# Kernel tuning notes

Hardware: AMD Instinct MI355X
Metric: run time of the kernel (lower is better)

The kernel has to match this reference:

```python
import jax, jax.numpy as jnp
import numpy as np

D = 768
H = 8
HD = D // H  # 96
DFF = 2048
EPS = 1e-5


def layernorm(x, g, b):
    mu = jnp.mean(x, axis=-1, keepdims=True)
    var = jnp.var(x, axis=-1, keepdims=True)
    return (x - mu) * jax.lax.rsqrt(var + EPS) * g + b


def setup_inputs() -> dict:
    key = jax.random.key(0)
    ks = jax.random.split(key, 12)
    B, L = 4, 1024
    s = lambda fan: 1.0 / np.sqrt(fan)
    return {
        "x": jax.random.normal(ks[0], (B, L, D), jnp.float32),
        "attn_bias": jax.random.normal(ks[1], (B, L, L), jnp.float32),
        "in_proj_w": jax.random.normal(ks[2], (3 * D, D), jnp.float32) * s(D),
        "in_proj_b": jnp.zeros((3 * D,), jnp.float32),
        "out_w": jax.random.normal(ks[3], (D, D), jnp.float32) * s(D),
        "out_b": jnp.zeros((D,), jnp.float32),
        "ff1_w": jax.random.normal(ks[4], (DFF, D), jnp.float32) * s(D),
        "ff1_b": jnp.zeros((DFF,), jnp.float32),
        "ff2_w": jax.random.normal(ks[5], (D, DFF), jnp.float32) * s(DFF),
        "ff2_b": jnp.zeros((D,), jnp.float32),
        "ln1_g": jnp.ones((D,), jnp.float32),
        "ln1_b": jnp.zeros((D,), jnp.float32),
        "ln2_g": jnp.ones((D,), jnp.float32),
        "ln2_b": jnp.zeros((D,), jnp.float32),
    }


def reference(x, attn_bias, in_proj_w, in_proj_b, out_w, out_b,
              ff1_w, ff1_b, ff2_w, ff2_b, ln1_g, ln1_b, ln2_g, ln2_b):
    B, L, _ = x.shape
    # combined QKV projection (torch nn.MultiheadAttention in_proj)
    qkv = x @ in_proj_w.T + in_proj_b  # [B,L,3D]
    q, k, v = jnp.split(qkv, 3, axis=-1)
    q = q.reshape(B, L, H, HD).transpose(0, 2, 1, 3)  # [B,H,L,hd]
    k = k.reshape(B, L, H, HD).transpose(0, 2, 1, 3)
    v = v.reshape(B, L, H, HD).transpose(0, 2, 1, 3)
    scale = 1.0 / np.sqrt(HD)
    scores = jnp.einsum('bhld,bhmd->bhlm', q, k) * scale + attn_bias[:, None, :, :]
    probs = jax.nn.softmax(scores, axis=-1)
    attn = jnp.einsum('bhlm,bhmd->bhld', probs, v)  # [B,H,L,hd]
    attn = attn.transpose(0, 2, 1, 3).reshape(B, L, D)
    attn = attn @ out_w.T + out_b
    x = layernorm(x + attn, ln1_g, ln1_b)
    h = jax.nn.gelu(x @ ff1_w.T + ff1_b, approximate=False) @ ff2_w.T + ff2_b
    x = layernorm(x + h, ln2_g, ln2_b)
    return x
```

## Files before the change

kernel.cpp:

```cpp
#include <hip/hip_runtime.h>

typedef __bf16 bf16x8 __attribute__((ext_vector_type(8)));
typedef float f32x4 __attribute__((ext_vector_type(4)));
typedef unsigned short u16x8 __attribute__((ext_vector_type(8)));
typedef short s16x4 __attribute__((ext_vector_type(4)));

__device__ __forceinline__ unsigned short f2b(float f) {
    union { float f; unsigned u; } v; v.f = f;
    unsigned r = (v.u + 0x7fffu + ((v.u >> 16) & 1u)) >> 16;
    return (unsigned short)r;
}

__device__ __forceinline__ void load_lds16(const void* g, void* l) {
    __builtin_amdgcn_global_load_lds(
        (const __attribute__((address_space(1))) unsigned int*)g,
        (__attribute__((address_space(3))) unsigned int*)l,
        16, 0, 0);
}

__global__ void cvt_kernel(const float* __restrict__ in, unsigned short* __restrict__ out, int n4) {
    int i = blockIdx.x * 256 + threadIdx.x;
    if (i < n4) {
        f32x4 v = ((const f32x4*)in)[i];
        s16x4 o;
        o.x = (short)f2b(v.x);
        o.y = (short)f2b(v.y);
        o.z = (short)f2b(v.z);
        o.w = (short)f2b(v.w);
        ((s16x4*)out)[i] = o;
    }
}

template <int BM, int BN, int EPI>
__global__ __launch_bounds__(512, 1)
void gemm_pipe(const unsigned short* __restrict__ A, const unsigned short* __restrict__ Bm,
               const float* __restrict__ bias, void* __restrict__ Cout,
               int M, int N, int K) {
    constexpr int ACH = BM / 8;
    constexpr int TC  = (BM + BN) / 8;
    constexpr int CPW = TC / 8;
    constexpr int MR = 4;
    constexpr int NR = BN / 64;
    constexpr int WN = BN / 4;
    constexpr int WSTR = (WN == 64) ? 72 : 36;
    constexpr int ABYTES = BM * 128;
    constexpr int BBYTES = BN * 128;
    constexpr int SMEM_BYTES = 3 * (ABYTES + BBYTES);
    static_assert(8 * 64 * WSTR * 4 <= SMEM_BYTES, "epilogue fits");
    __shared__ char smem[SMEM_BYTES];

    const int tid = threadIdx.x, lane = tid & 63, wid = tid >> 6;
    const int l15 = lane & 15, lq = lane >> 4;
    const int wr = wid >> 2, wc = wid & 3;

    const int nwg = gridDim.x * gridDim.y;
    int bid = blockIdx.y * gridDim.x + blockIdx.x;
    bid = (bid & 7) * (nwg >> 3) + (bid >> 3);
    const int bx = bid % gridDim.x, by = bid / gridDim.x;
    const int m0 = by * BM, n0 = bx * BN;

    const int srow = lane >> 3;
    const int scol = ((lane & 7) ^ srow) * 8;

    f32x4 acc[MR][NR];
#pragma unroll
    for (int i = 0; i < MR; i++)
#pragma unroll
        for (int j = 0; j < NR; j++) acc[i][j] = 0.0f;

    auto stage = [&](int buf, int kt) {
        const int kb = kt * 64;
#pragma unroll
        for (int i = 0; i < CPW; ++i) {
            const int c = wid * CPW + i;
            if (c < ACH) {
                load_lds16(A + (size_t)(m0 + c * 8 + srow) * K + kb + scol,
                           smem + buf * ABYTES + c * 1024);
            } else {
                load_lds16(Bm + (size_t)(n0 + (c - ACH) * 8 + srow) * K + kb + scol,
                           smem + 3 * ABYTES + buf * BBYTES + (c - ACH) * 1024);
            }
        }
    };

    auto compute = [&](int buf) {
#pragma unroll
        for (int kc = 0; kc < 2; ++kc) {
            const int cb = kc * 64;
            const int sw = (l15 & 7) << 4;
            bf16x8 af[MR], bf[NR];
#pragma unroll
            for (int mi = 0; mi < MR; mi++) {
                const int row = wr * 64 + mi * 16 + l15;
                af[mi] = *(const bf16x8*)(smem + buf * ABYTES + row * 128 + ((cb + lq * 16) ^ sw));
            }
#pragma unroll
            for (int ni = 0; ni < NR; ni++) {
                const int row = wc * WN + ni * 16 + l15;
                bf[ni] = *(const bf16x8*)(smem + 3 * ABYTES + buf * BBYTES + row * 128 + ((cb + lq * 16) ^ sw));
            }
#pragma unroll
            for (int mi = 0; mi < MR; mi++)
#pragma unroll
                for (int ni = 0; ni < NR; ni++)
                    acc[mi][ni] = __builtin_amdgcn_mfma_f32_16x16x32_bf16(af[mi], bf[ni], acc[mi][ni], 0, 0, 0);
        }
    };

    const int nkt = K / 64;
    stage(0, 0);
    stage(1, 1);
    stage(2, 2);
    int cur = 0;
    for (int t = 0; t < nkt; ++t) {
        if (t <= nkt - 3)      asm volatile("s_waitcnt vmcnt(12)" ::: "memory");
        else if (t == nkt - 2) asm volatile("s_waitcnt vmcnt(6)" ::: "memory");
        else                   asm volatile("s_waitcnt vmcnt(0)" ::: "memory");
        __builtin_amdgcn_s_barrier();
        asm volatile("" ::: "memory");
        compute(cur);
        asm volatile("" ::: "memory");
        __builtin_amdgcn_s_barrier();
        if (t + 3 < nkt) stage(cur, t + 3);
        cur = (cur == 2) ? 0 : cur + 1;
    }

    float* ew = (float*)(smem + wid * 64 * WSTR * 4);
#pragma unroll
    for (int mi = 0; mi < MR; mi++) {
#pragma unroll
        for (int ni = 0; ni < NR; ni++) {
            const int cl = ni * 16 + l15;
            const float bv = bias[n0 + wc * WN + cl];
#pragma unroll
            for (int r = 0; r < 4; r++) {
                const int rl = mi * 16 + lq * 4 + r;
                float v = acc[mi][ni][r] + bv;
                if constexpr (EPI == 2) {
                    v = 0.5f * v * (1.0f + erff(v * 0.7071067811865475f));
                }
                ew[rl * WSTR + (cl ^ (lq << 3))] = v;
            }
        }
    }
    asm volatile("s_waitcnt lgkmcnt(0)" ::: "memory");

    if constexpr (WN == 64) {
        const int r8 = lane >> 3, c8 = lane & 7;
#pragma unroll
        for (int j = 0; j < 8; j++) {
            const int row = r8 + 8 * j;
            const int po = c8 ^ ((row >> 2) & 3);
            f32x4 a = *(const f32x4*)(ew + row * WSTR + po * 8);
            f32x4 b = *(const f32x4*)(ew + row * WSTR + po * 8 + 4);
            const int grow = m0 + wr * 64 + row;
            const int gcol = n0 + wc * WN + c8 * 8;
            if constexpr (EPI == 1) {
                *(f32x4*)&((float*)Cout)[(size_t)grow * N + gcol] = a;
                *(f32x4*)&((float*)Cout)[(size_t)grow * N + gcol + 4] = b;
            } else {
                u16x8 p;
#pragma unroll
                for (int e = 0; e < 4; e++) { p[e] = f2b(a[e]); p[e + 4] = f2b(b[e]); }
                *(u16x8*)&((unsigned short*)Cout)[(size_t)grow * N + gcol] = p;
            }
        }
    } else {
        const int r8 = lane >> 2, c8 = lane & 3;
#pragma unroll
        for (int j = 0; j < 4; j++) {
            const int row = r8 + 16 * j;
            const int po = c8 ^ ((row >> 2) & 3);
            f32x4 a = *(const f32x4*)(ew + row * WSTR + po * 8);
            f32x4 b = *(const f32x4*)(ew + row * WSTR + po * 8 + 4);
            const int grow = m0 + wr * 64 + row;
            const int gcol = n0 + wc * WN + c8 * 8;
            if constexpr (EPI == 1) {
                *(f32x4*)&((float*)Cout)[(size_t)grow * N + gcol] = a;
                *(f32x4*)&((float*)Cout)[(size_t)grow * N + gcol + 4] = b;
            } else {
                u16x8 p;
#pragma unroll
                for (int e = 0; e < 4; e++) { p[e] = f2b(a[e]); p[e + 4] = f2b(b[e]); }
                *(u16x8*)&((unsigned short*)Cout)[(size_t)grow * N + gcol] = p;
            }
        }
    }
}

__global__ __launch_bounds__(256, 2)
void attn_kernel(const unsigned short* __restrict__ qkv,
                 const float* __restrict__ bias,
                 unsigned short* __restrict__ out) {
    const int L = 1024, TD = 2304, HD = 96;
    const int qt = blockIdx.x, h = blockIdx.y, b = blockIdx.z;
    const int tid = threadIdx.x, lane = tid & 63, wid = tid >> 6;
    const int l15 = lane & 15, lq = lane >> 4;
    const int q0 = qt * 64;
    const float scale = 0.10206207261596576f;

    __shared__ unsigned short Ks[64][104];
    __shared__ unsigned short Vt[96][72];
    __shared__ unsigned short Ps[4][16][72];
    __shared__ float Ot[4][16][100];

    bf16x8 qf[3];
    const int qrow = q0 + wid * 16 + l15;
#pragma unroll
    for (int kc = 0; kc < 3; kc++)
        qf[kc] = *(const bf16x8*)(qkv + (size_t)(b * L + qrow) * TD + h * HD + kc * 32 + lq * 8);

    f32x4 o[6];
#pragma unroll
    for (int df = 0; df < 6; df++) o[df] = 0.0f;
    float mrow[4] = {-1e30f, -1e30f, -1e30f, -1e30f};
    float lrow[4] = {0.f, 0.f, 0.f, 0.f};

    for (int kv0 = 0; kv0 < L; kv0 += 64) {
#pragma unroll
        for (int i = 0; i < 3; i++) {
            int c = i * 256 + tid;
            int row = c / 12, cc = c % 12;
            *(f32x4*)&Ks[row][cc * 8] =
                *(const f32x4*)(qkv + (size_t)(b * L + kv0 + row) * TD + 768 + h * HD + cc * 8);
        }
#pragma unroll
        for (int i = 0; i < 3; i++) {
            int dblk = i * 4 + wid;
            int m = lane;
            u16x8 v = *(const u16x8*)(qkv + (size_t)(b * L + kv0 + m) * TD + 1536 + h * HD + dblk * 8);
#pragma unroll
            for (int j = 0; j < 8; j++) Vt[dblk * 8 + j][m] = v[j];
        }
        __syncthreads();

        f32x4 s[4];
#pragma unroll
        for (int nf = 0; nf < 4; nf++) s[nf] = 0.0f;
#pragma unroll
        for (int kc = 0; kc < 3; kc++) {
#pragma unroll
            for (int nf = 0; nf < 4; nf++) {
                bf16x8 kf = *(const bf16x8*)&Ks[nf * 16 + l15][kc * 32 + lq * 8];
                s[nf] = __builtin_amdgcn_mfma_f32_16x16x32_bf16(qf[kc], kf, s[nf], 0, 0, 0);
            }
        }
#pragma unroll
        for (int nf = 0; nf < 4; nf++) {
            int colg = kv0 + nf * 16 + l15;
#pragma unroll
            for (int r = 0; r < 4; r++) {
                int rowg = q0 + wid * 16 + lq * 4 + r;
                s[nf][r] = s[nf][r] * scale + bias[((size_t)b * L + rowg) * L + colg];
            }
        }
        float pm[4];
#pragma unroll
        for (int r = 0; r < 4; r++) {
            float mx = fmaxf(fmaxf(s[0][r], s[1][r]), fmaxf(s[2][r], s[3][r]));
#pragma unroll
            for (int d = 1; d < 16; d <<= 1) mx = fmaxf(mx, __shfl_xor(mx, d, 64));
            pm[r] = mx;
        }
        float alpha[4];
#pragma unroll
        for (int r = 0; r < 4; r++) {
            float mn = fmaxf(mrow[r], pm[r]);
            alpha[r] = __expf(mrow[r] - mn);
            mrow[r] = mn;
        }
        float rs[4] = {0.f, 0.f, 0.f, 0.f};
#pragma unroll
        for (int nf = 0; nf < 4; nf++)
#pragma unroll
            for (int r = 0; r < 4; r++) {
                float p = __expf(s[nf][r] - mrow[r]);
                s[nf][r] = p;
                rs[r] += p;
            }
#pragma unroll
        for (int r = 0; r < 4; r++) {
#pragma unroll
            for (int d = 1; d < 16; d <<= 1) rs[r] += __shfl_xor(rs[r], d, 64);
            lrow[r] = lrow[r] * alpha[r] + rs[r];
        }
#pragma unroll
        for (int nf = 0; nf < 4; nf++)
#pragma unroll
            for (int r = 0; r < 4; r++)
                Ps[wid][lq * 4 + r][nf * 16 + l15] = f2b(s[nf][r]);
#pragma unroll
        for (int df = 0; df < 6; df++)
#pragma unroll
            for (int r = 0; r < 4; r++) o[df][r] *= alpha[r];
        asm volatile("s_waitcnt lgkmcnt(0)" ::: "memory");
#pragma unroll
        for (int kc = 0; kc < 2; kc++) {
            bf16x8 pf = *(const bf16x8*)&Ps[wid][l15][kc * 32 + lq * 8];
#pragma unroll
            for (int df = 0; df < 6; df++) {
                bf16x8 vf = *(const bf16x8*)&Vt[df * 16 + l15][kc * 32 + lq * 8];
                o[df] = __builtin_amdgcn_mfma_f32_16x16x32_bf16(pf, vf, o[df], 0, 0, 0);
            }
        }
        __syncthreads();
    }

#pragma unroll
    for (int r = 0; r < 4; r++) {
        float inv = 1.0f / lrow[r];
        const int rl = lq * 4 + r;
#pragma unroll
        for (int df = 0; df < 6; df++) {
            const int cl = df * 16 + l15;
            Ot[wid][rl][cl ^ (lq << 3)] = o[df][r] * inv;
        }
    }
    asm volatile("s_waitcnt lgkmcnt(0)" ::: "memory");
    {
        const int r = lane >> 2, c8 = lane & 3;
        const int rowg = q0 + wid * 16 + r;
#pragma unroll
        for (int it = 0; it < 3; it++) {
            const int oc = c8 + 4 * it;
            const int po = oc ^ ((r >> 2) & 3);
            f32x4 a = *(const f32x4*)&Ot[wid][r][po * 8];
            f32x4 bb = *(const f32x4*)&Ot[wid][r][po * 8 + 4];
            u16x8 p;
#pragma unroll
            for (int e = 0; e < 4; e++) { p[e] = f2b(a[e]); p[e + 4] = f2b(bb[e]); }
            *(u16x8*)&out[((size_t)b * L + rowg) * 768 + h * 96 + oc * 8] = p;
        }
    }
}

template <int WRITE_B>
__global__ __launch_bounds__(256, 4)
void ln_kernel(const float* __restrict__ x, const float* __restrict__ res,
               const float* __restrict__ g, const float* __restrict__ bvec,
               float* __restrict__ outf, unsigned short* __restrict__ outb) {
    const int Dm = 768;
    int row = blockIdx.x;
    int tid = threadIdx.x;
    f32x4 v = {0.f, 0.f, 0.f, 0.f};
    float sum = 0.f, sq = 0.f;
    if (tid < 192) {
        f32x4 xv = ((const f32x4*)(x + (size_t)row * Dm))[tid];
        f32x4 rv = ((const f32x4*)(res + (size_t)row * Dm))[tid];
        v = xv + rv;
        sum = v.x + v.y + v.z + v.w;
        sq = v.x * v.x + v.y * v.y + v.z * v.z + v.w * v.w;
    }
#pragma unroll
    for (int d = 1; d < 64; d <<= 1) {
        sum += __shfl_xor(sum, d, 64);
        sq += __shfl_xor(sq, d, 64);
    }
    __shared__ float ps[8];
    int lane = tid & 63, wid = tid >> 6;
    if (lane == 0) { ps[wid] = sum; ps[wid + 4] = sq; }
    __syncthreads();
    sum = ps[0] + ps[1] + ps[2] + ps[3];
    sq = ps[4] + ps[5] + ps[6] + ps[7];
    float mu = sum * (1.0f / 768.0f);
    float var = sq * (1.0f / 768.0f) - mu * mu;
    float rsg = rsqrtf(var + 1e-5f);
    if (tid < 192) {
        f32x4 gv = ((const f32x4*)g)[tid];
        f32x4 bv = ((const f32x4*)bvec)[tid];
        f32x4 ov;
#pragma unroll
        for (int e = 0; e < 4; e++) ov[e] = (v[e] - mu) * rsg * gv[e] + bv[e];
        ((f32x4*)(outf + (size_t)row * Dm))[tid] = ov;
        if constexpr (WRITE_B) {
            s16x4 pb;
#pragma unroll
            for (int e = 0; e < 4; e++) pb[e] = (short)f2b(ov[e]);
            ((s16x4*)(outb + (size_t)row * Dm))[tid] = pb;
        }
    }
}

extern "C" void kernel_launch(void* const* d_in, const int* in_sizes, int n_in,
                              void* d_out, int out_size, void* d_ws, size_t ws_size,
                              hipStream_t stream) {
    (void)in_sizes; (void)n_in; (void)out_size; (void)ws_size;
    const float* x         = (const float*)d_in[0];
    const float* attn_bias = (const float*)d_in[1];
    const float* in_proj_w = (const float*)d_in[2];
    const float* in_proj_b = (const float*)d_in[3];
    const float* out_w     = (const float*)d_in[4];
    const float* out_b     = (const float*)d_in[5];
    const float* ff1_w     = (const float*)d_in[6];
    const float* ff1_b     = (const float*)d_in[7];
    const float* ff2_w     = (const float*)d_in[8];
    const float* ff2_b     = (const float*)d_in[9];
    const float* ln1_g     = (const float*)d_in[10];
    const float* ln1_b     = (const float*)d_in[11];
    const float* ln2_g     = (const float*)d_in[12];
    const float* ln2_b     = (const float*)d_in[13];

    const int NTOK = 4096;
    char* ws = (char*)d_ws;
    size_t off = 0;
    auto alloc = [&](size_t bytes) { void* p = ws + off; off += (bytes + 255) & ~(size_t)255; return p; };
    unsigned short* xb    = (unsigned short*)alloc((size_t)NTOK * 768 * 2);
    unsigned short* wqkv  = (unsigned short*)alloc((size_t)2304 * 768 * 2);
    unsigned short* wout  = (unsigned short*)alloc((size_t)768 * 768 * 2);
    unsigned short* wff1  = (unsigned short*)alloc((size_t)2048 * 768 * 2);
    unsigned short* wff2  = (unsigned short*)alloc((size_t)768 * 2048 * 2);
    unsigned short* qkvb  = (unsigned short*)alloc((size_t)NTOK * 2304 * 2);
    unsigned short* attnb = (unsigned short*)alloc((size_t)NTOK * 768 * 2);
    float*          aproj = (float*)alloc((size_t)NTOK * 768 * 4);
    float*          x1f   = (float*)alloc((size_t)NTOK * 768 * 4);
    unsigned short* x1b   = (unsigned short*)alloc((size_t)NTOK * 768 * 2);
    unsigned short* h1b  = qkvb;
    float*          ff2o = aproj;

    cvt_kernel<<<dim3((NTOK * 768 / 4) / 256), 256, 0, stream>>>(x, xb, NTOK * 768 / 4);
    cvt_kernel<<<dim3((2304 * 768 / 4) / 256), 256, 0, stream>>>(in_proj_w, wqkv, 2304 * 768 / 4);
    cvt_kernel<<<dim3((768 * 768 / 4) / 256), 256, 0, stream>>>(out_w, wout, 768 * 768 / 4);
    cvt_kernel<<<dim3((2048 * 768 / 4) / 256), 256, 0, stream>>>(ff1_w, wff1, 2048 * 768 / 4);
    cvt_kernel<<<dim3((768 * 2048 / 4) / 256), 256, 0, stream>>>(ff2_w, wff2, 768 * 2048 / 4);

    gemm_pipe<128, 256, 0><<<dim3(2304 / 256, NTOK / 128), 512, 0, stream>>>(xb, wqkv, in_proj_b, qkvb, NTOK, 2304, 768);
    attn_kernel<<<dim3(16, 8, 4), 256, 0, stream>>>(qkvb, attn_bias, attnb);
    gemm_pipe<128, 128, 1><<<dim3(768 / 128, NTOK / 128), 512, 0, stream>>>(attnb, wout, out_b, aproj, NTOK, 768, 768);
    ln_kernel<1><<<dim3(NTOK), 256, 0, stream>>>(x, aproj, ln1_g, ln1_b, x1f, x1b);
    gemm_pipe<128, 256, 2><<<dim3(2048 / 256, NTOK / 128), 512, 0, stream>>>(x1b, wff1, ff1_b, h1b, NTOK, 2048, 768);
    gemm_pipe<128, 128, 1><<<dim3(768 / 128, NTOK / 128), 512, 0, stream>>>(h1b, wff2, ff2_b, ff2o, NTOK, 768, 2048);
    ln_kernel<0><<<dim3(NTOK), 256, 0, stream>>>(x1f, ff2o, ln2_g, ln2_b, (float*)d_out, nullptr);
}
```

Measured before the change: 180.7 us.

## Replace LDS-pipelined GEMM with register-direct GEMM and fuse conversion kernels

Replaces the 512-thread GEMM, which staged tiles into LDS with a triple-buffered global_load_lds pipeline, with a 256-thread kernel where each wave loads its MFMA fragments straight from global memory into registers. Tiles are smaller, so more blocks launch and two blocks can share a CU. The five fp32-to-bf16 conversion launches are merged into one kernel with hardcoded segment offsets. The GEMM change gives up the cross-wave LDS data reuse and the explicit latency hiding, relying on cache hits and occupancy instead.

Result: slower. 329.8 us (+82.5%).

```diff
diff --git a/kernel.cpp b/kernel.cpp
--- a/kernel.cpp
+++ b/kernel.cpp
@@ -11,56 +11,57 @@
     return (unsigned short)r;
 }
 
-__device__ __forceinline__ void load_lds16(const void* g, void* l) {
-    __builtin_amdgcn_global_load_lds(
-        (const __attribute__((address_space(1))) unsigned int*)g,
-        (__attribute__((address_space(3))) unsigned int*)l,
-        16, 0, 0);
-}
-
-__global__ void cvt_kernel(const float* __restrict__ in, unsigned short* __restrict__ out, int n4) {
+__global__ void cvt5_kernel(const float* __restrict__ s0, const float* __restrict__ s1,
+                            const float* __restrict__ s2, const float* __restrict__ s3,
+                            const float* __restrict__ s4,
+                            unsigned short* __restrict__ d0, unsigned short* __restrict__ d1,
+                            unsigned short* __restrict__ d2, unsigned short* __restrict__ d3,
+                            unsigned short* __restrict__ d4) {
     int i = blockIdx.x * 256 + threadIdx.x;
-    if (i < n4) {
-        f32x4 v = ((const f32x4*)in)[i];
-        s16x4 o;
-        o.x = (short)f2b(v.x);
-        o.y = (short)f2b(v.y);
-        o.z = (short)f2b(v.z);
-        o.w = (short)f2b(v.w);
-        ((s16x4*)out)[i] = o;
-    }
-}
-
-template <int BM, int BN, int EPI>
-__global__ __launch_bounds__(512, 1)
-void gemm_pipe(const unsigned short* __restrict__ A, const unsigned short* __restrict__ Bm,
-               const float* __restrict__ bias, void* __restrict__ Cout,
-               int M, int N, int K) {
-    constexpr int ACH = BM / 8;
-    constexpr int TC  = (BM + BN) / 8;
-    constexpr int CPW = TC / 8;
-    constexpr int MR = 4;
-    constexpr int NR = BN / 64;
-    constexpr int WN = BN / 4;
+    const float* s; unsigned short* d; int off;
+    if (i < 786432)       { s = s0; d = d0; off = 0; }
+    else if (i < 1228800) { s = s1; d = d1; off = 786432; }
+    else if (i < 1376256) { s = s2; d = d2; off = 1228800; }
+    else if (i < 1769472) { s = s3; d = d3; off = 1376256; }
+    else                  { s = s4; d = d4; off = 1769472; }
+    i -= off;
+    f32x4 v = ((const f32x4*)s)[i];
+    s16x4 o;
+    o.x = (short)f2b(v.x);
+    o.y = (short)f2b(v.y);
+    o.z = (short)f2b(v.z);
+    o.w = (short)f2b(v.w);
+    ((s16x4*)d)[i] = o;
+}
+
+template <int WM, int WN, int EPI>
+__global__ __launch_bounds__(256, 2)
+void gemm_reg(const unsigned short* __restrict__ A, const unsigned short* __restrict__ Bm,
+              const float* __restrict__ bias, void* __restrict__ Cout,
+              int M, int N, int K) {
+    constexpr int MR = WM / 16, NR = WN / 16;
+    constexpr int BM = 2 * WM, BN = 2 * WN;
     constexpr int WSTR = (WN == 64) ? 72 : 36;
-    constexpr int ABYTES = BM * 128;
-    constexpr int BBYTES = BN * 128;
-    constexpr int SMEM_BYTES = 3 * (ABYTES + BBYTES);
-    static_assert(8 * 64 * WSTR * 4 <= SMEM_BYTES, "epilogue fits");
-    __shared__ char smem[SMEM_BYTES];
+    constexpr int CROWS = 32;
+    constexpr int NCH = WM / CROWS;
+    __shared__ float ews[4][CROWS][WSTR];
 
     const int tid = threadIdx.x, lane = tid & 63, wid = tid >> 6;
     const int l15 = lane & 15, lq = lane >> 4;
-    const int wr = wid >> 2, wc = wid & 3;
+    const int wr = wid >> 1, wc = wid & 1;
 
     const int nwg = gridDim.x * gridDim.y;
     int bid = blockIdx.y * gridDim.x + blockIdx.x;
     bid = (bid & 7) * (nwg >> 3) + (bid >> 3);
     const int bx = bid % gridDim.x, by = bid / gridDim.x;
-    const int m0 = by * BM, n0 = bx * BN;
-
-    const int srow = lane >> 3;
-    const int scol = ((lane & 7) ^ srow) * 8;
+    const int m0 = by * BM + wr * WM, n0 = bx * BN + wc * WN;
+
+    const unsigned short* Ar[MR];
+    const unsigned short* Br[NR];
+#pragma unroll
+    for (int mi = 0; mi < MR; mi++) Ar[mi] = A + (size_t)(m0 + mi * 16 + l15) * K + lq * 8;
+#pragma unroll
+    for (int ni = 0; ni < NR; ni++) Br[ni] = Bm + (size_t)(n0 + ni * 16 + l15) * K + lq * 8;
 
     f32x4 acc[MR][NR];
 #pragma unroll
@@ -68,121 +69,83 @@
 #pragma unroll
         for (int j = 0; j < NR; j++) acc[i][j] = 0.0f;
 
-    auto stage = [&](int buf, int kt) {
-        const int kb = kt * 64;
-#pragma unroll
-        for (int i = 0; i < CPW; ++i) {
-            const int c = wid * CPW + i;
-            if (c < ACH) {
-                load_lds16(A + (size_t)(m0 + c * 8 + srow) * K + kb + scol,
-                           smem + buf * ABYTES + c * 1024);
-            } else {
-                load_lds16(Bm + (size_t)(n0 + (c - ACH) * 8 + srow) * K + kb + scol,
-                           smem + 3 * ABYTES + buf * BBYTES + (c - ACH) * 1024);
-            }
-        }
-    };
-
-    auto compute = [&](int buf) {
-#pragma unroll
-        for (int kc = 0; kc < 2; ++kc) {
-            const int cb = kc * 64;
-            const int sw = (l15 & 7) << 4;
-            bf16x8 af[MR], bf[NR];
-#pragma unroll
-            for (int mi = 0; mi < MR; mi++) {
-                const int row = wr * 64 + mi * 16 + l15;
-                af[mi] = *(const bf16x8*)(smem + buf * ABYTES + row * 128 + ((cb + lq * 16) ^ sw));
-            }
+#pragma unroll 2
+    for (int k = 0; k < K; k += 32) {
+        bf16x8 af[MR], bf[NR];
+#pragma unroll
+        for (int mi = 0; mi < MR; mi++) af[mi] = *(const bf16x8*)(Ar[mi] + k);
+#pragma unroll
+        for (int ni = 0; ni < NR; ni++) bf[ni] = *(const bf16x8*)(Br[ni] + k);
+#pragma unroll
+        for (int mi = 0; mi < MR; mi++)
+#pragma unroll
+            for (int ni = 0; ni < NR; ni++)
+                acc[mi][ni] = __builtin_amdgcn_mfma_f32_16x16x32_bf16(af[mi], bf[ni], acc[mi][ni], 0, 0, 0);
+    }
+
+    float bv[NR];
+#pragma unroll
+    for (int ni = 0; ni < NR; ni++) bv[ni] = bias[n0 + ni * 16 + l15];
+
+#pragma unroll
+    for (int ch = 0; ch < NCH; ch++) {
+#pragma unroll
+        for (int mi2 = 0; mi2 < CROWS / 16; mi2++) {
+            const int mi = ch * (CROWS / 16) + mi2;
 #pragma unroll
             for (int ni = 0; ni < NR; ni++) {
-                const int row = wc * WN + ni * 16 + l15;
-                bf[ni] = *(const bf16x8*)(smem + 3 * ABYTES + buf * BBYTES + row * 128 + ((cb + lq * 16) ^ sw));
-            }
-#pragma unroll
-            for (int mi = 0; mi < MR; mi++)
-#pragma unroll
-                for (int ni = 0; ni < NR; ni++)
-                    acc[mi][ni] = __builtin_amdgcn_mfma_f32_16x16x32_bf16(af[mi], bf[ni], acc[mi][ni], 0, 0, 0);
-        }
-    };
-
-    const int nkt = K / 64;
-    stage(0, 0);
-    stage(1, 1);
-    stage(2, 2);
-    int cur = 0;
-    for (int t = 0; t < nkt; ++t) {
-        if (t <= nkt - 3)      asm volatile("s_waitcnt vmcnt(12)" ::: "memory");
-        else if (t == nkt - 2) asm volatile("s_waitcnt vmcnt(6)" ::: "memory");
-        else                   asm volatile("s_waitcnt vmcnt(0)" ::: "memory");
-        __builtin_amdgcn_s_barrier();
-        asm volatile("" ::: "memory");
-        compute(cur);
-        asm volatile("" ::: "memory");
-        __builtin_amdgcn_s_barrier();
-        if (t + 3 < nkt) stage(cur, t + 3);
-        cur = (cur == 2) ? 0 : cur + 1;
-    }
-
-    float* ew = (float*)(smem + wid * 64 * WSTR * 4);
-#pragma unroll
-    for (int mi = 0; mi < MR; mi++) {
-#pragma unroll
-        for (int ni = 0; ni < NR; ni++) {
-            const int cl = ni * 16 + l15;
-            const float bv = bias[n0 + wc * WN + cl];
-#pragma unroll
-            for (int r = 0; r < 4; r++) {
-                const int rl = mi * 16 + lq * 4 + r;
-                float v = acc[mi][ni][r] + bv;
-                if constexpr (EPI == 2) {
-                    v = 0.5f * v * (1.0f + erff(v * 0.7071067811865475f));
+                const int cl = ni * 16 + l15;
+#pragma unroll
+                for (int r = 0; r < 4; r++) {
+                    const int rl = mi2 * 16 + lq * 4 + r;
+                    float v = acc[mi][ni][r] + bv[ni];
+                    if constexpr (EPI == 2) {
+                        v = 0.5f * v * (1.0f + erff(v * 0.7071067811865475f));
+                    }
+                    ews[wid][rl][cl ^ (lq << 3)] = v;
                 }
-                ew[rl * WSTR + (cl ^ (lq << 3))] = v;
-            }
-        }
-    }
-    asm volatile("s_waitcnt lgkmcnt(0)" ::: "memory");
-
-    if constexpr (WN == 64) {
-        const int r8 = lane >> 3, c8 = lane & 7;
-#pragma unroll
-        for (int j = 0; j < 8; j++) {
-            const int row = r8 + 8 * j;
-            const int po = c8 ^ ((row >> 2) & 3);
-            f32x4 a = *(const f32x4*)(ew + row * WSTR + po * 8);
-            f32x4 b = *(const f32x4*)(ew + row * WSTR + po * 8 + 4);
-            const int grow = m0 + wr * 64 + row;
-            const int gcol = n0 + wc * WN + c8 * 8;
-            if constexpr (EPI == 1) {
-                *(f32x4*)&((float*)Cout)[(size_t)grow * N + gcol] = a;
-                *(f32x4*)&((float*)Cout)[(size_t)grow * N + gcol + 4] = b;
-            } else {
-                u16x8 p;
-#pragma unroll
-                for (int e = 0; e < 4; e++) { p[e] = f2b(a[e]); p[e + 4] = f2b(b[e]); }
-                *(u16x8*)&((unsigned short*)Cout)[(size_t)grow * N + gcol] = p;
-            }
-        }
-    } else {
-        const int r8 = lane >> 2, c8 = lane & 3;
-#pragma unroll
-        for (int j = 0; j < 4; j++) {
-            const int row = r8 + 16 * j;
-            const int po = c8 ^ ((row >> 2) & 3);
-            f32x4 a = *(const f32x4*)(ew + row * WSTR + po * 8);
-            f32x4 b = *(const f32x4*)(ew + row * WSTR + po * 8 + 4);
-            const int grow = m0 + wr * 64 + row;
-            const int gcol = n0 + wc * WN + c8 * 8;
-            if constexpr (EPI == 1) {
-                *(f32x4*)&((float*)Cout)[(size_t)grow * N + gcol] = a;
-                *(f32x4*)&((float*)Cout)[(size_t)grow * N + gcol + 4] = b;
-            } else {
-                u16x8 p;
-#pragma unroll
-                for (int e = 0; e < 4; e++) { p[e] = f2b(a[e]); p[e + 4] = f2b(b[e]); }
-                *(u16x8*)&((unsigned short*)Cout)[(size_t)grow * N + gcol] = p;
+            }
+        }
+        asm volatile("s_waitcnt lgkmcnt(0)" ::: "memory");
+        if constexpr (WN == 64) {
+            const int r8 = lane >> 3, c8 = lane & 7;
+#pragma unroll
+            for (int j = 0; j < 4; j++) {
+                const int row = r8 + 8 * j;
+                const int po = c8 ^ ((row >> 2) & 3);
+                f32x4 a = *(const f32x4*)&ews[wid][row][po * 8];
+                f32x4 b = *(const f32x4*)&ews[wid][row][po * 8 + 4];
+                const int grow = m0 + ch * CROWS + row;
+                const int gcol = n0 + c8 * 8;
+                if constexpr (EPI == 1) {
+                    *(f32x4*)&((float*)Cout)[(size_t)grow * N + gcol] = a;
+                    *(f32x4*)&((float*)Cout)[(size_t)grow * N + gcol + 4] = b;
+                } else {
+                    u16x8 p;
+#pragma unroll
+                    for (int e = 0; e < 4; e++) { p[e] = f2b(a[e]); p[e + 4] = f2b(b[e]); }
+                    *(u16x8*)&((unsigned short*)Cout)[(size_t)grow * N + gcol] = p;
+                }
+            }
+        } else {
+            const int r8 = lane >> 2, c8 = lane & 3;
+#pragma unroll
+            for (int j = 0; j < 2; j++) {
+                const int row = r8 + 16 * j;
+                const int po = c8 ^ ((row >> 2) & 3);
+                f32x4 a = *(const f32x4*)&ews[wid][row][po * 8];
+                f32x4 b = *(const f32x4*)&ews[wid][row][po * 8 + 4];
+                const int grow = m0 + ch * CROWS + row;
+                const int gcol = n0 + c8 * 8;
+                if constexpr (EPI == 1) {
+                    *(f32x4*)&((float*)Cout)[(size_t)grow * N + gcol] = a;
+                    *(f32x4*)&((float*)Cout)[(size_t)grow * N + gcol + 4] = b;
+                } else {
+                    u16x8 p;
+#pragma unroll
+                    for (int e = 0; e < 4; e++) { p[e] = f2b(a[e]); p[e + 4] = f2b(b[e]); }
+                    *(u16x8*)&((unsigned short*)Cout)[(size_t)grow * N + gcol] = p;
+                }
             }
         }
     }
@@ -417,17 +380,14 @@
     unsigned short* h1b  = qkvb;
     float*          ff2o = aproj;
 
-    cvt_kernel<<<dim3((NTOK * 768 / 4) / 256), 256, 0, stream>>>(x, xb, NTOK * 768 / 4);
-    cvt_kernel<<<dim3((2304 * 768 / 4) / 256), 256, 0, stream>>>(in_proj_w, wqkv, 2304 * 768 / 4);
-    cvt_kernel<<<dim3((768 * 768 / 4) / 256), 256, 0, stream>>>(out_w, wout, 768 * 768 / 4);
-    cvt_kernel<<<dim3((2048 * 768 / 4) / 256), 256, 0, stream>>>(ff1_w, wff1, 2048 * 768 / 4);
-    cvt_kernel<<<dim3((768 * 2048 / 4) / 256), 256, 0, stream>>>(ff2_w, wff2, 768 * 2048 / 4);
-
-    gemm_pipe<128, 256, 0><<<dim3(2304 / 256, NTOK / 128), 512, 0, stream>>>(xb, wqkv, in_proj_b, qkvb, NTOK, 2304, 768);
+    cvt5_kernel<<<dim3(8448), 256, 0, stream>>>(x, in_proj_w, out_w, ff1_w, ff2_w,
+                                                xb, wqkv, wout, wff1, wff2);
+
+    gemm_reg<64, 64, 0><<<dim3(2304 / 128, NTOK / 128), 256, 0, stream>>>(xb, wqkv, in_proj_b, qkvb, NTOK, 2304, 768);
     attn_kernel<<<dim3(16, 8, 4), 256, 0, stream>>>(qkvb, attn_bias, attnb);
-    gemm_pipe<128, 128, 1><<<dim3(768 / 128, NTOK / 128), 512, 0, stream>>>(attnb, wout, out_b, aproj, NTOK, 768, 768);
+    gemm_reg<32, 64, 1><<<dim3(768 / 128, NTOK / 64), 256, 0, stream>>>(attnb, wout, out_b, aproj, NTOK, 768, 768);
     ln_kernel<1><<<dim3(NTOK), 256, 0, stream>>>(x, aproj, ln1_g, ln1_b, x1f, x1b);
-    gemm_pipe<128, 256, 2><<<dim3(2048 / 256, NTOK / 128), 512, 0, stream>>>(x1b, wff1, ff1_b, h1b, NTOK, 2048, 768);
-    gemm_pipe<128, 128, 1><<<dim3(768 / 128, NTOK / 128), 512, 0, stream>>>(h1b, wff2, ff2_b, ff2o, NTOK, 768, 2048);
+    gemm_reg<64, 64, 2><<<dim3(2048 / 128, NTOK / 128), 256, 0, stream>>>(x1b, wff1, ff1_b, h1b, NTOK, 2048, 768);
+    gemm_reg<32, 64, 1><<<dim3(768 / 128, NTOK / 64), 256, 0, stream>>>(h1b, wff2, ff2_b, ff2o, NTOK, 768, 2048);
     ln_kernel<0><<<dim3(NTOK), 256, 0, stream>>>(x1f, ff2o, ln2_g, ln2_b, (float*)d_out, nullptr);
 }
```
